# Kernel optimization log

Measured on AMD Instinct MI355X. Metric: run time of the kernel, lower is better.

Reference implementation:

```python
import jax, jax.numpy as jnp
import numpy as np

# Dimensions (match init_kwargs / input_specs)
B, T, HW, K, J = 8192, 64, 8, 64, 3
FILT_LEN = 8
NEG_SLOPE = 0.001
DWT_OUT_LEN = 84  # lo(14) + hi1(35) + hi2(21) + hi3(14)

# db4 analysis filters (pywt dec_lo / dec_hi)
DB4_LO = np.array([-0.010597401784997278, 0.032883011666982945,
                   0.030841381835986965, -0.18703481171888114,
                   -0.02798376941698385, 0.6308807679295904,
                   0.7148465705525415, 0.23037781330885523], dtype=np.float32)
DB4_HI = np.array([-0.23037781330885523, 0.7148465705525415,
                   -0.6308807679295904, -0.02798376941698385,
                   0.18703481171888114, 0.030841381835986965,
                   0.032883011666982945, -0.010597401784997278], dtype=np.float32)
# pytorch_wavelets stores filters reversed and uses conv1d (cross-correlation)
_H = jnp.asarray(np.ascontiguousarray(np.stack([DB4_LO[::-1], DB4_HI[::-1]])[:, None, :]))  # [2,1,8]


def _afb1d(x):
    # Single-level analysis filter bank along last axis, reflect padding, stride 2.
    # x: [N, n] -> (lo, hi) each [N, floor((n+7)/2)]
    n = x.shape[-1]
    out = (n + FILT_LEN - 1) // 2
    p = 2 * (out - 1) - n + FILT_LEN
    xp = jnp.pad(x, ((0, 0), (p // 2, (p + 1) // 2)), mode='reflect')
    y = jax.lax.conv_general_dilated(xp[:, None, :], _H, (2,), 'VALID')  # [N,2,out]
    return y[:, 0], y[:, 1]


def _dwt(x):
    # J-level DWT; concat [lo_J, hi_1, hi_2, ..., hi_J] along last axis -> [N, 84]
    lo, his = x, []
    for _ in range(J):
        lo, hi = _afb1d(lo)
        his.append(hi)
    return jnp.concatenate([lo] + his, axis=-1)


def setup_inputs() -> dict:
    key = jax.random.key(0)
    k1, k2 = jax.random.split(key)
    x = jax.random.normal(k1, (B, 1, T, HW, HW), dtype=jnp.float32)
    fan_in = DWT_OUT_LEN * HW * HW
    conv_w = jax.random.normal(k2, (K, DWT_OUT_LEN, HW, HW), dtype=jnp.float32) / np.sqrt(fan_in).astype(np.float32)
    conv_b = jnp.zeros((K,), dtype=jnp.float32)
    return {"x": x, "conv_w": conv_w, "conv_b": conv_b}


def reference(x, conv_w, conv_b):
    # x: [B,1,T,H,W]; time_interval=1 and spatial_maxpool_size=1 -> no-ops.
    b = x.shape[0]
    # DWT along time for every (batch, spatial) signal, fully batched.
    sig = x[:, 0].transpose(0, 2, 3, 1).reshape(b * HW * HW, T)  # [B*H*W, T]
    coeffs = _dwt(sig).reshape(b, HW, HW, DWT_OUT_LEN)           # [B,H,W,84]
    # Conv3d with kernel covering the full (84,8,8) volume == one GEMM per output channel.
    feat = jnp.einsum('bhwt,kthw->bk', coeffs, conv_w) + conv_b  # [B,K]
    # Dropout3d in eval mode is identity; LeakyReLU then flatten -> [B, K]
    return jnp.where(feat >= 0, feat, NEG_SLOPE * feat)
```

## Files before the change

kernel.cpp:

```cpp
#include <hip/hip_runtime.h>
#include <hip/hip_bf16.h>

typedef __attribute__((ext_vector_type(4))) float floatx4;
typedef __attribute__((ext_vector_type(8))) short shortx8;

__device__ __constant__ float DLO[8] = {
    -0.010597401784997278f, 0.032883011666982945f,
     0.030841381835986965f, -0.18703481171888114f,
    -0.02798376941698385f,  0.6308807679295904f,
     0.7148465705525415f,   0.23037781330885523f};
__device__ __constant__ float DHI[8] = {
    -0.23037781330885523f,  0.7148465705525415f,
    -0.6308807679295904f,  -0.02798376941698385f,
     0.18703481171888114f,  0.030841381835986965f,
     0.032883011666982945f, -0.010597401784997278f};

__device__ __forceinline__ unsigned short f2bf_rne(float f) {
  unsigned u = __builtin_bit_cast(unsigned, f);
  unsigned r = (u + 0x7FFFu + ((u >> 16) & 1u)) >> 16;
  return (unsigned short)r;
}

template <int N, int OUT>
__device__ __forceinline__ void afb(const float* x, float* lo, float* hi) {
#pragma unroll
  for (int m = 0; m < OUT; ++m) {
    float aL = 0.f, aH = 0.f;
#pragma unroll
    for (int i = 0; i < 8; ++i) {
      int s = 2 * m + 1 - i;
      s = (s < 0) ? -s : s;
      s = (s >= N) ? (2 * N - 2 - s) : s;
      float v = x[s];
      aL = fmaf(DLO[i], v, aL);
      aH = fmaf(DHI[i], v, aH);
    }
    lo[m] = aL; hi[m] = aH;
  }
}

__global__ void build_M_kernel(float* __restrict__ M) {
  const int i = threadIdx.x;
  float sig[64];
#pragma unroll
  for (int t = 0; t < 64; ++t) sig[t] = (t == i) ? 1.f : 0.f;
  float lo1[35], hi1[35], lo2[21], hi2[21], lo3[14], hi3[14];
  afb<64, 35>(sig, lo1, hi1);
  afb<35, 21>(lo1, lo2, hi2);
  afb<21, 14>(lo2, lo3, hi3);
#pragma unroll
  for (int t = 0; t < 14; ++t) M[t * 64 + i] = lo3[t];
#pragma unroll
  for (int t = 0; t < 35; ++t) M[(14 + t) * 64 + i] = hi1[t];
#pragma unroll
  for (int t = 0; t < 21; ++t) M[(49 + t) * 64 + i] = hi2[t];
#pragma unroll
  for (int t = 0; t < 14; ++t) M[(70 + t) * 64 + i] = hi3[t];
}

__global__ __launch_bounds__(256) void build_w2_kernel(
    const float* __restrict__ M, const float* __restrict__ cw,
    unsigned short* __restrict__ W2) {
  __shared__ float Ml[84 * 64];
  __shared__ float Cl[84 * 64];
  const int k = blockIdx.x;
  const float* cwk = cw + (size_t)k * (84 * 64);
  for (int idx = threadIdx.x; idx < 84 * 64; idx += 256) {
    Ml[idx] = M[idx];
    Cl[idx] = cwk[idx];
  }
  __syncthreads();
  const int tp  = blockIdx.y * 16 + (threadIdx.x >> 4);
  const int hw0 = (threadIdx.x & 15) * 4;
  float a0 = 0.f, a1 = 0.f, a2 = 0.f, a3 = 0.f;
#pragma unroll 4
  for (int t = 0; t < 84; ++t) {
    const float mv = Ml[t * 64 + tp];
    const float4 cv = *(const float4*)&Cl[t * 64 + hw0];
    a0 = fmaf(mv, cv.x, a0);
    a1 = fmaf(mv, cv.y, a1);
    a2 = fmaf(mv, cv.z, a2);
    a3 = fmaf(mv, cv.w, a3);
  }
  uint2 pk;
  pk.x = (unsigned)f2bf_rne(a0) | ((unsigned)f2bf_rne(a1) << 16);
  pk.y = (unsigned)f2bf_rne(a2) | ((unsigned)f2bf_rne(a3) << 16);
  *(uint2*)(W2 + (size_t)k * 4096 + tp * 64 + hw0) = pk;
}

#define BM 32
#define BN 64
#define BK 128
#define LDK 136
#define NITER 32

__global__ __launch_bounds__(512) void gemm_kernel(
    const float* __restrict__ A, const unsigned short* __restrict__ W2,
    const float* __restrict__ bias, float* __restrict__ out) {
  __shared__ alignas(16) short As[2][BM * LDK];
  __shared__ alignas(16) short Bs[2][BN * LDK];

  const int tid = threadIdx.x;
  const int b0 = blockIdx.x * BM;

  const int ar = tid >> 4;
  const int ac = (tid & 15) * 8;
  const int bn = tid >> 3;
  const int bc = (tid & 7) * 16;

  const float* aptr = A + (size_t)(b0 + ar) * 4096 + ac;
  const unsigned short* bptr = W2 + (size_t)bn * 4096 + bc;

  const int lane = tid & 63;
  const int wave = tid >> 6;
  const int mt = wave >> 2;
  const int nt = wave & 3;
  const int frow = lane & 15;
  const int fk = (lane >> 4) * 8;

  floatx4 acc = {0.f, 0.f, 0.f, 0.f};

  float4 a0_0 = *(const float4*)(aptr + 0);
  float4 a1_0 = *(const float4*)(aptr + 4);
  uint4  b0_0 = *(const uint4*)(bptr + 0);
  uint4  b1_0 = *(const uint4*)(bptr + 8);
  float4 a0_1 = *(const float4*)(aptr + BK);
  float4 a1_1 = *(const float4*)(aptr + BK + 4);
  uint4  b0_1 = *(const uint4*)(bptr + BK);
  uint4  b1_1 = *(const uint4*)(bptr + BK + 8);

#define GSTEP(S, I)                                                          \
  do {                                                                       \
    shortx8 av;                                                              \
    av[0] = (short)f2bf_rne(a0_##S.x); av[1] = (short)f2bf_rne(a0_##S.y);    \
    av[2] = (short)f2bf_rne(a0_##S.z); av[3] = (short)f2bf_rne(a0_##S.w);    \
    av[4] = (short)f2bf_rne(a1_##S.x); av[5] = (short)f2bf_rne(a1_##S.y);    \
    av[6] = (short)f2bf_rne(a1_##S.z); av[7] = (short)f2bf_rne(a1_##S.w);    \
    *(shortx8*)&As[S][ar * LDK + ac] = av;                                   \
    *(uint4*)&Bs[S][bn * LDK + bc] = b0_##S;                                 \
    *(uint4*)&Bs[S][bn * LDK + bc + 8] = b1_##S;                             \
    __asm__ __volatile__("s_waitcnt lgkmcnt(0)\n\ts_barrier" ::: "memory");  \
    if ((I) + 2 < NITER) {                                                   \
      const int c2 = ((I) + 2) * BK;                                         \
      a0_##S = *(const float4*)(aptr + c2);                                  \
      a1_##S = *(const float4*)(aptr + c2 + 4);                              \
      b0_##S = *(const uint4*)(bptr + c2);                                   \
      b1_##S = *(const uint4*)(bptr + c2 + 8);                               \
    }                                                                        \
    _Pragma("unroll")                                                        \
    for (int kk = 0; kk < 4; ++kk) {                                         \
      shortx8 af = *(const shortx8*)&As[S][(mt * 16 + frow) * LDK + kk * 32 + fk]; \
      shortx8 bf = *(const shortx8*)&Bs[S][(nt * 16 + frow) * LDK + kk * 32 + fk]; \
      acc = __builtin_amdgcn_mfma_f32_16x16x32_bf16(af, bf, acc, 0, 0, 0);   \
    }                                                                        \
  } while (0)

  for (int i = 0; i < NITER; i += 2) {
    GSTEP(0, i);
    GSTEP(1, i + 1);
  }
#undef GSTEP

  const int ocol = nt * 16 + (lane & 15);
  const int orow0 = b0 + mt * 16 + (lane >> 4) * 4;
  const float bv = bias[ocol];
#pragma unroll
  for (int r = 0; r < 4; ++r) {
    float v = acc[r] + bv;
    out[(size_t)(orow0 + r) * 64 + ocol] = (v >= 0.f) ? v : 1.0e-3f * v;
  }
}

extern "C" void kernel_launch(void* const* d_in, const int* in_sizes, int n_in,
                              void* d_out, int out_size, void* d_ws, size_t ws_size,
                              hipStream_t stream) {
  const float* x      = (const float*)d_in[0];
  const float* conv_w = (const float*)d_in[1];
  const float* conv_b = (const float*)d_in[2];
  float* out = (float*)d_out;

  float* Mws = (float*)d_ws;
  unsigned short* W2 = (unsigned short*)((char*)d_ws + 32768);

  build_M_kernel<<<1, 64, 0, stream>>>(Mws);
  build_w2_kernel<<<dim3(64, 4), 256, 0, stream>>>(Mws, conv_w, W2);
  gemm_kernel<<<256, 512, 0, stream>>>(x, W2, conv_b, out);
}
```

Baseline: 202.7 us.

## Fuse DWT matrix build into weight prep and halve GEMM row tile

The separate single-block kernel that built the 84x64 DWT matrix is folded into the weight-folding kernel: each block recomputes the matrix directly into shared memory, which removes one launch and a global round trip. The GEMM tile shrinks from 32 to 16 batch rows with 256 threads, giving 512 blocks instead of 256 to spread over more compute units. The cost is that each block now reloads the full bf16 weight matrix for fewer rows, doubling weight traffic per output, and each weight-prep block carries redundant serial DWT work.

```diff
diff --git a/kernel.cpp b/kernel.cpp
--- a/kernel.cpp
+++ b/kernel.cpp
@@ -1,5 +1,4 @@
 #include <hip/hip_runtime.h>
-#include <hip/hip_bf16.h>
 
 typedef __attribute__((ext_vector_type(4))) float floatx4;
 typedef __attribute__((ext_vector_type(8))) short shortx8;
@@ -39,39 +38,37 @@
   }
 }
 
-__global__ void build_M_kernel(float* __restrict__ M) {
-  const int i = threadIdx.x;
-  float sig[64];
-#pragma unroll
-  for (int t = 0; t < 64; ++t) sig[t] = (t == i) ? 1.f : 0.f;
-  float lo1[35], hi1[35], lo2[21], hi2[21], lo3[14], hi3[14];
-  afb<64, 35>(sig, lo1, hi1);
-  afb<35, 21>(lo1, lo2, hi2);
-  afb<21, 14>(lo2, lo3, hi3);
-#pragma unroll
-  for (int t = 0; t < 14; ++t) M[t * 64 + i] = lo3[t];
-#pragma unroll
-  for (int t = 0; t < 35; ++t) M[(14 + t) * 64 + i] = hi1[t];
-#pragma unroll
-  for (int t = 0; t < 21; ++t) M[(49 + t) * 64 + i] = hi2[t];
-#pragma unroll
-  for (int t = 0; t < 14; ++t) M[(70 + t) * 64 + i] = hi3[t];
-}
-
-__global__ __launch_bounds__(256) void build_w2_kernel(
-    const float* __restrict__ M, const float* __restrict__ cw,
-    unsigned short* __restrict__ W2) {
+__global__ __launch_bounds__(256) void build_w2_fused(
+    const float* __restrict__ cw, unsigned short* __restrict__ W2) {
   __shared__ float Ml[84 * 64];
   __shared__ float Cl[84 * 64];
   const int k = blockIdx.x;
+  const int tid = threadIdx.x;
+
+  if (tid < 64) {
+    const int i = tid;
+    float sig[64];
+#pragma unroll
+    for (int t = 0; t < 64; ++t) sig[t] = (t == i) ? 1.f : 0.f;
+    float lo1[35], hi1[35], lo2[21], hi2[21], lo3[14], hi3[14];
+    afb<64, 35>(sig, lo1, hi1);
+    afb<35, 21>(lo1, lo2, hi2);
+    afb<21, 14>(lo2, lo3, hi3);
+#pragma unroll
+    for (int t = 0; t < 14; ++t) Ml[t * 64 + i] = lo3[t];
+#pragma unroll
+    for (int t = 0; t < 35; ++t) Ml[(14 + t) * 64 + i] = hi1[t];
+#pragma unroll
+    for (int t = 0; t < 21; ++t) Ml[(49 + t) * 64 + i] = hi2[t];
+#pragma unroll
+    for (int t = 0; t < 14; ++t) Ml[(70 + t) * 64 + i] = hi3[t];
+  }
   const float* cwk = cw + (size_t)k * (84 * 64);
-  for (int idx = threadIdx.x; idx < 84 * 64; idx += 256) {
-    Ml[idx] = M[idx];
-    Cl[idx] = cwk[idx];
-  }
+  for (int idx = tid; idx < 84 * 64; idx += 256) Cl[idx] = cwk[idx];
   __syncthreads();
-  const int tp  = blockIdx.y * 16 + (threadIdx.x >> 4);
-  const int hw0 = (threadIdx.x & 15) * 4;
+
+  const int tp  = blockIdx.y * 16 + (tid >> 4);
+  const int hw0 = (tid & 15) * 4;
   float a0 = 0.f, a1 = 0.f, a2 = 0.f, a3 = 0.f;
 #pragma unroll 4
   for (int t = 0; t < 84; ++t) {
@@ -88,13 +85,13 @@
   *(uint2*)(W2 + (size_t)k * 4096 + tp * 64 + hw0) = pk;
 }
 
-#define BM 32
+#define BM 16
 #define BN 64
 #define BK 128
 #define LDK 136
 #define NITER 32
 
-__global__ __launch_bounds__(512) void gemm_kernel(
+__global__ __launch_bounds__(256) void gemm_kernel(
     const float* __restrict__ A, const unsigned short* __restrict__ W2,
     const float* __restrict__ bias, float* __restrict__ out) {
   __shared__ alignas(16) short As[2][BM * LDK];
@@ -105,29 +102,30 @@
 
   const int ar = tid >> 4;
   const int ac = (tid & 15) * 8;
-  const int bn = tid >> 3;
-  const int bc = (tid & 7) * 16;
+  const int bn = tid >> 2;
+  const int bc = (tid & 3) * 32;
 
   const float* aptr = A + (size_t)(b0 + ar) * 4096 + ac;
   const unsigned short* bptr = W2 + (size_t)bn * 4096 + bc;
 
   const int lane = tid & 63;
   const int wave = tid >> 6;
-  const int mt = wave >> 2;
-  const int nt = wave & 3;
   const int frow = lane & 15;
   const int fk = (lane >> 4) * 8;
 
   floatx4 acc = {0.f, 0.f, 0.f, 0.f};
 
-  float4 a0_0 = *(const float4*)(aptr + 0);
-  float4 a1_0 = *(const float4*)(aptr + 4);
-  uint4  b0_0 = *(const uint4*)(bptr + 0);
-  uint4  b1_0 = *(const uint4*)(bptr + 8);
-  float4 a0_1 = *(const float4*)(aptr + BK);
-  float4 a1_1 = *(const float4*)(aptr + BK + 4);
-  uint4  b0_1 = *(const uint4*)(bptr + BK);
-  uint4  b1_1 = *(const uint4*)(bptr + BK + 8);
+  float4 a0_0, a1_0, a0_1, a1_1;
+  uint4  bq_0[4], bq_1[4];
+  a0_0 = *(const float4*)(aptr + 0);
+  a1_0 = *(const float4*)(aptr + 4);
+  a0_1 = *(const float4*)(aptr + BK);
+  a1_1 = *(const float4*)(aptr + BK + 4);
+#pragma unroll
+  for (int j = 0; j < 4; ++j) {
+    bq_0[j] = *(const uint4*)(bptr + j * 8);
+    bq_1[j] = *(const uint4*)(bptr + BK + j * 8);
+  }
 
 #define GSTEP(S, I)                                                          \
   do {                                                                       \
@@ -137,20 +135,24 @@
     av[4] = (short)f2bf_rne(a1_##S.x); av[5] = (short)f2bf_rne(a1_##S.y);    \
     av[6] = (short)f2bf_rne(a1_##S.z); av[7] = (short)f2bf_rne(a1_##S.w);    \
     *(shortx8*)&As[S][ar * LDK + ac] = av;                                   \
-    *(uint4*)&Bs[S][bn * LDK + bc] = b0_##S;                                 \
-    *(uint4*)&Bs[S][bn * LDK + bc + 8] = b1_##S;                             \
+    *(uint4*)&Bs[S][bn * LDK + bc] = bq_##S[0];                              \
+    *(uint4*)&Bs[S][bn * LDK + bc + 8] = bq_##S[1];                          \
+    *(uint4*)&Bs[S][bn * LDK + bc + 16] = bq_##S[2];                         \
+    *(uint4*)&Bs[S][bn * LDK + bc + 24] = bq_##S[3];                         \
     __asm__ __volatile__("s_waitcnt lgkmcnt(0)\n\ts_barrier" ::: "memory");  \
     if ((I) + 2 < NITER) {                                                   \
       const int c2 = ((I) + 2) * BK;                                         \
       a0_##S = *(const float4*)(aptr + c2);                                  \
       a1_##S = *(const float4*)(aptr + c2 + 4);                              \
-      b0_##S = *(const uint4*)(bptr + c2);                                   \
-      b1_##S = *(const uint4*)(bptr + c2 + 8);                               \
+      _Pragma("unroll")                                                      \
+      for (int j = 0; j < 4; ++j) {                                          \
+        bq_##S[j] = *(const uint4*)(bptr + c2 + j * 8);                      \
+      }                                                                      \
     }                                                                        \
     _Pragma("unroll")                                                        \
     for (int kk = 0; kk < 4; ++kk) {                                         \
-      shortx8 af = *(const shortx8*)&As[S][(mt * 16 + frow) * LDK + kk * 32 + fk]; \
-      shortx8 bf = *(const shortx8*)&Bs[S][(nt * 16 + frow) * LDK + kk * 32 + fk]; \
+      shortx8 af = *(const shortx8*)&As[S][frow * LDK + kk * 32 + fk];       \
+      shortx8 bf = *(const shortx8*)&Bs[S][(wave * 16 + frow) * LDK + kk * 32 + fk]; \
       acc = __builtin_amdgcn_mfma_f32_16x16x32_bf16(af, bf, acc, 0, 0, 0);   \
     }                                                                        \
   } while (0)
@@ -161,8 +163,8 @@
   }
 #undef GSTEP
 
-  const int ocol = nt * 16 + (lane & 15);
-  const int orow0 = b0 + mt * 16 + (lane >> 4) * 4;
+  const int ocol = wave * 16 + (lane & 15);
+  const int orow0 = b0 + (lane >> 4) * 4;
   const float bv = bias[ocol];
 #pragma unroll
   for (int r = 0; r < 4; ++r) {
@@ -179,10 +181,8 @@
   const float* conv_b = (const float*)d_in[2];
   float* out = (float*)d_out;
 
-  float* Mws = (float*)d_ws;
-  unsigned short* W2 = (unsigned short*)((char*)d_ws + 32768);
+  unsigned short* W2 = (unsigned short*)d_ws;
 
-  build_M_kernel<<<1, 64, 0, stream>>>(Mws);
-  build_w2_kernel<<<dim3(64, 4), 256, 0, stream>>>(Mws, conv_w, W2);
-  gemm_kernel<<<256, 512, 0, stream>>>(x, W2, conv_b, out);
+  build_w2_fused<<<dim3(64, 4), 256, 0, stream>>>(conv_w, W2);
+  gemm_kernel<<<512, 256, 0, stream>>>(x, W2, conv_b, out);
 }
```

Result: slower. 265.6 us (+31.0%).
